# Optimization experiments

Hardware: AMD Instinct MI355X
Metric: run time of the kernel (lower is better)

Reference implementation:

```python
import jax, jax.numpy as jnp
import numpy as np

D_MODEL = 1024
HEADS = 16
D_HEAD = D_MODEL // HEADS
CAUSAL = True


def setup_inputs() -> dict:
    key = jax.random.key(0)
    ks = jax.random.split(key, 11)
    B, L = 4, 2048
    s = 1.0 / np.sqrt(D_MODEL)
    inp = {
        'q': jax.random.normal(ks[0], (B, L, D_MODEL), jnp.float32),
        'k': jax.random.normal(ks[1], (B, L, D_MODEL), jnp.float32),
        'v': jax.random.normal(ks[2], (B, L, D_MODEL), jnp.float32),
        'Wq': jax.random.normal(ks[3], (D_MODEL, D_MODEL), jnp.float32) * s,
        'bq': jnp.zeros((D_MODEL,), jnp.float32),
        'Wk': jax.random.normal(ks[4], (D_MODEL, D_MODEL), jnp.float32) * s,
        'bk': jnp.zeros((D_MODEL,), jnp.float32),
        'Wv': jax.random.normal(ks[5], (D_MODEL, D_MODEL), jnp.float32) * s,
        'bv': jnp.zeros((D_MODEL,), jnp.float32),
        'Wo': jax.random.normal(ks[6], (D_MODEL, D_MODEL), jnp.float32) * s,
        'bo': jnp.zeros((D_MODEL,), jnp.float32),
    }
    return inp


def _split(x):
    B, L, _ = x.shape
    return x.reshape(B, L, HEADS, D_HEAD).transpose(0, 2, 1, 3)  # [B,H,L,Dh]


def reference(q, k, v, Wq, bq, Wk, bk, Wv, bv, Wo, bo):
    qh = _split(q @ Wq + bq)
    kh = _split(k @ Wk + bk)
    vh = _split(v @ Wv + bv)
    scores = jnp.einsum('bhqd,bhkd->bhqk', qh, kh) / jnp.sqrt(jnp.float32(D_HEAD))
    if CAUSAL:
        Lq, Lk = q.shape[1], k.shape[1]
        mask = jnp.triu(jnp.ones((Lq, Lk), bool), k=1)
        scores = jnp.where(mask[None, None], -jnp.inf, scores)
    attn = jax.nn.softmax(scores, axis=-1)
    out = jnp.einsum('bhqk,bhkd->bhqd', attn, vh)
    B, H, L, Dh = out.shape
    out = out.transpose(0, 2, 1, 3).reshape(B, L, H * Dh)
    return out @ Wo + bo
```

## Files before the change

kernel.cpp:

```cpp
#include <hip/hip_runtime.h>

#define DM 1024
#define HEADS 16
#define DH 64
#define BB 4
#define LL 2048
#define MROWS (BB * LL)

typedef __bf16 bf16x8 __attribute__((ext_vector_type(8)));
typedef float f32x4 __attribute__((ext_vector_type(4)));
typedef float f32x16 __attribute__((ext_vector_type(16)));

__device__ __forceinline__ unsigned short f2bf(float f) {
  __bf16 h = (__bf16)f;
  return __builtin_bit_cast(unsigned short, h);
}
__device__ __forceinline__ unsigned int pack2(float a, float b) {
  return (unsigned int)f2bf(a) | ((unsigned int)f2bf(b) << 16);
}

__device__ __forceinline__ void gload16(const unsigned short* g, unsigned short* l) {
  __builtin_amdgcn_global_load_lds(
      (const __attribute__((address_space(1))) unsigned int*)(const void*)g,
      (__attribute__((address_space(3))) unsigned int*)(void*)l, 16, 0, 0);
}

__global__ __launch_bounds__(256) void transpose_w_kernel(
    const float* __restrict__ W0, const float* __restrict__ W1,
    const float* __restrict__ W2, const float* __restrict__ W3,
    unsigned short* __restrict__ T0, unsigned short* __restrict__ T1,
    unsigned short* __restrict__ T2, unsigned short* __restrict__ T3) {
  const float* Wt[4] = {W0, W1, W2, W3};
  unsigned short* Tt[4] = {T0, T1, T2, T3};
  const float* W = Wt[blockIdx.z];
  unsigned short* WT = Tt[blockIdx.z];
  __shared__ float tile[32][33];
  const int tx = threadIdx.x & 31;
  const int ty = threadIdx.x >> 5;
  const int x0 = blockIdx.x * 32;
  const int y0 = blockIdx.y * 32;
#pragma unroll
  for (int i = 0; i < 32; i += 8)
    tile[ty + i][tx] = W[(size_t)(y0 + ty + i) * DM + x0 + tx];
  __syncthreads();
#pragma unroll
  for (int i = 0; i < 32; i += 8)
    WT[(size_t)(x0 + ty + i) * DM + y0 + tx] = f2bf(tile[tx][ty + i]);
}

__global__ __launch_bounds__(256) void cvt_bf16_kernel(
    const float* __restrict__ x, unsigned short* __restrict__ y) {
  const size_t i = ((size_t)blockIdx.x * 256 + threadIdx.x) * 8;
  float4 a = *(const float4*)(x + i);
  float4 b = *(const float4*)(x + i + 4);
  uint4 p = {pack2(a.x, a.y), pack2(a.z, a.w), pack2(b.x, b.y), pack2(b.z, b.w)};
  *(uint4*)(y + i) = p;
}

__global__ __launch_bounds__(256) void cvt3_bf16_kernel(
    const float* __restrict__ q, const float* __restrict__ k,
    const float* __restrict__ v, unsigned short* __restrict__ Xq,
    unsigned short* __restrict__ Xk, unsigned short* __restrict__ Xv) {
  const int z = blockIdx.y;
  const float* x = (z == 0) ? q : (z == 1) ? k : v;
  unsigned short* y = (z == 0) ? Xq : (z == 1) ? Xk : Xv;
  const size_t i = ((size_t)blockIdx.x * 256 + threadIdx.x) * 8;
  float4 a = *(const float4*)(x + i);
  float4 b = *(const float4*)(x + i + 4);
  uint4 p = {pack2(a.x, a.y), pack2(a.z, a.w), pack2(b.x, b.y), pack2(b.z, b.w)};
  *(uint4*)(y + i) = p;
}

template <int OUTMODE>
__device__ __forceinline__ void gemm_body64(
    const unsigned short* __restrict__ A, const unsigned short* __restrict__ BT,
    const float* __restrict__ bias, void* __restrict__ Cptr, float scale) {
  constexpr int K = DM, N = DM;
  __shared__ unsigned short As[128 * 64];
  __shared__ unsigned short Bs[128 * 64];
  const int t = threadIdx.x;
  const int lane = t & 63;
  const int w = t >> 6;
  const int wr = w >> 1, wc = w & 1;
  const int fr = lane & 15, kg = lane >> 4;

  const int flat = blockIdx.y * gridDim.x + blockIdx.x;
  const int cpx = (gridDim.x * gridDim.y) >> 3;
  const int swz = (flat & 7) * cpx + (flat >> 3);
  const int m0 = (swz / gridDim.x) * 128;
  const int n0 = (swz % gridDim.x) * 128;

  const int srow = t >> 3, scol = (t & 7) * 8;

  f32x4 acc[4][4] = {};

  for (int kt = 0; kt < K / 64; ++kt) {
    const int k0 = kt * 64;
#pragma unroll
    for (int i = 0; i < 4; i++) {
      gload16(A + (size_t)(m0 + i * 32 + srow) * K + k0 + scol,
              &As[(i * 256 + t) * 8]);
      gload16(BT + (size_t)(n0 + i * 32 + srow) * K + k0 + scol,
              &Bs[(i * 256 + t) * 8]);
    }
    __syncthreads();

#pragma unroll
    for (int ks = 0; ks < 2; ks++) {
      bf16x8 af[4], bfr[4];
#pragma unroll
      for (int i = 0; i < 4; i++)
        af[i] = *(const bf16x8*)&As[(wr * 64 + i * 16 + fr) * 64 + ks * 32 + kg * 8];
#pragma unroll
      for (int i = 0; i < 4; i++)
        bfr[i] = *(const bf16x8*)&Bs[(wc * 64 + i * 16 + fr) * 64 + ks * 32 + kg * 8];
#pragma unroll
      for (int i = 0; i < 4; i++)
#pragma unroll
        for (int j = 0; j < 4; j++)
          acc[i][j] = __builtin_amdgcn_mfma_f32_16x16x32_bf16(af[i], bfr[j], acc[i][j], 0, 0, 0);
    }
    __syncthreads();
  }

#pragma unroll
  for (int j = 0; j < 4; j++) {
    const int gcol = n0 + wc * 64 + j * 16 + fr;
    const float bv = bias[gcol];
    const int h = gcol >> 6, dh = gcol & 63;
#pragma unroll
    for (int i = 0; i < 4; i++) {
      const int grow0 = m0 + wr * 64 + i * 16 + kg * 4;
      if (OUTMODE == 2) {
        const int b = grow0 >> 11, l = grow0 & 2047;
        uint2 pk;
        pk.x = pack2(acc[i][j][0] + bv, acc[i][j][1] + bv);
        pk.y = pack2(acc[i][j][2] + bv, acc[i][j][3] + bv);
        *(uint2*)((unsigned short*)Cptr +
                  ((size_t)((b * HEADS + h) * DH + dh)) * LL + l) = pk;
      } else {
#pragma unroll
        for (int r = 0; r < 4; r++) {
          const int grow2 = grow0 + r;
          if (OUTMODE == 0) {
            const float val = (acc[i][j][r] + bv) * scale;
            const int b = grow2 >> 11, l = grow2 & 2047;
            ((unsigned short*)Cptr)[(((size_t)(b * HEADS + h) * LL + l) << 6) + dh] = f2bf(val);
          } else {
            ((float*)Cptr)[(size_t)grow2 * N + gcol] = acc[i][j][r] + bv;
          }
        }
      }
    }
  }
}

#define QSCALE 0.18033688011112042f

__global__ __launch_bounds__(256) void qkv_gemm_kernel(
    const unsigned short* __restrict__ A0, size_t strideA,
    const unsigned short* __restrict__ WT0,
    const float* __restrict__ bq, const float* __restrict__ bk,
    const float* __restrict__ bv, unsigned short* __restrict__ O0, int zoff) {
  const int z = (int)blockIdx.z + zoff;
  const unsigned short* A = A0 + (size_t)z * strideA;
  const unsigned short* BT = WT0 + (size_t)z * DM * DM;
  const float* bias = (z == 0) ? bq : (z == 1) ? bk : bv;
  unsigned short* C = O0 + (size_t)z * MROWS * DM;
  if (z == 2)
    gemm_body64<2>(A, BT, bias, C, 1.0f);
  else
    gemm_body64<0>(A, BT, bias, C, (z == 0) ? QSCALE : 1.0f);
}

__global__ __launch_bounds__(256) void oproj_gemm_kernel(
    const unsigned short* __restrict__ Oc, const unsigned short* __restrict__ WoT,
    const float* __restrict__ bo, float* __restrict__ out) {
  gemm_body64<1>(Oc, WoT, bo, out, 1.0f);
}

#define PAD 76
__global__ __launch_bounds__(256, 4) void attn_kernel(
    const unsigned short* __restrict__ Qh, const unsigned short* __restrict__ Kh,
    const unsigned short* __restrict__ VhT, unsigned short* __restrict__ O) {
  __shared__ unsigned short Ks[2][64][PAD];
  __shared__ unsigned short VTs[2][64][PAD];
  const int t = threadIdx.x, lane = t & 63, w = t >> 6;
  const int lo5 = lane & 31, hi = lane >> 5;

  const int f = (int)(blockIdx.y * gridDim.x + blockIdx.x);
  const int l = f >> 8;
  const int c = f & 255;
  const int xcd = c & 7, j = c >> 3;
  const int bh = xcd * 8 + (j & 7);
  const int sub = j >> 3;
  const int qi = (l == 0) ? sub : (l == 1) ? 7 - sub : (l == 2) ? 8 + sub : 15 - sub;

  const size_t base = (size_t)bh * LL * DH;
  const unsigned short* Kb = Kh + base;
  const unsigned short* Vb = VhT + base;

  const int rA = t >> 3, kA = (t & 7) * 8;
  const int rB = rA + 32;

  const int b = bh >> 4, h = bh & 15;

  const int q0 = qi * 128;
  const int qrow = q0 + w * 32 + lo5;

  bf16x8 qf[4];
  {
    const unsigned short* Qb = Qh + base + (size_t)qrow * DH + hi * 8;
#pragma unroll
    for (int kc = 0; kc < 4; kc++) qf[kc] = *(const bf16x8*)(Qb + kc * 16);
  }

  float m_run = -INFINITY, l_run = 0.f;
  f32x16 oacc[2] = {};

  const int ntiles = 2 * (qi + 1);
  const int my_last = (q0 + w * 32 + 31) >> 6;

  uint4 kr0 = *(const uint4*)(Kb + (size_t)rA * DH + kA);
  uint4 kr1 = *(const uint4*)(Kb + (size_t)rB * DH + kA);
  uint4 vr0 = *(const uint4*)(Vb + (size_t)rA * LL + kA);
  uint4 vr1 = *(const uint4*)(Vb + (size_t)rB * LL + kA);
  *(uint4*)&Ks[0][rA][kA] = kr0;
  *(uint4*)&Ks[0][rB][kA] = kr1;
  *(uint4*)&VTs[0][rA][kA] = vr0;
  *(uint4*)&VTs[0][rB][kA] = vr1;

  for (int jt = 0; jt < ntiles; ++jt) {
    const int cur = jt & 1;
    if (jt + 1 < ntiles) {
      const int kv1 = (jt + 1) * 64;
      kr0 = *(const uint4*)(Kb + (size_t)(kv1 + rA) * DH + kA);
      kr1 = *(const uint4*)(Kb + (size_t)(kv1 + rB) * DH + kA);
      vr0 = *(const uint4*)(Vb + (size_t)rA * LL + kv1 + kA);
      vr1 = *(const uint4*)(Vb + (size_t)rB * LL + kv1 + kA);
    }
    __syncthreads();

    if (jt <= my_last) {
      f32x16 s2[2] = {};
      __builtin_amdgcn_s_setprio(1);
#pragma unroll
      for (int tt = 0; tt < 2; tt++)
#pragma unroll
        for (int kc = 0; kc < 4; kc++) {
          bf16x8 kf = *(const bf16x8*)&Ks[cur][tt * 32 + lo5][kc * 16 + hi * 8];
          s2[tt] = __builtin_amdgcn_mfma_f32_32x32x16_bf16(kf, qf[kc], s2[tt], 0, 0, 0);
        }
      __builtin_amdgcn_s_setprio(0);

      const int kv0 = jt * 64;
      if (kv0 + 63 > q0 + w * 32) {
        const int thr = qrow - kv0 - 4 * hi;
#pragma unroll
        for (int tt = 0; tt < 2; tt++)
#pragma unroll
          for (int i = 0; i < 16; i++) {
            const int kvoff = tt * 32 + (i & 3) + 8 * (i >> 2);
            s2[tt][i] = (kvoff > thr) ? -1e30f : s2[tt][i];
          }
      }

      float mx;
      {
        float m8[8];
#pragma unroll
        for (int i = 0; i < 8; i++)
          m8[i] = fmaxf(fmaxf(s2[0][i], s2[0][i + 8]), fmaxf(s2[1][i], s2[1][i + 8]));
        const float a3 = fmaxf(fmaxf(m8[0], m8[1]), m8[2]);
        const float b3 = fmaxf(fmaxf(m8[3], m8[4]), m8[5]);
        const float c3 = fmaxf(m8[6], m8[7]);
        mx = fmaxf(fmaxf(a3, b3), c3);
      }
      mx = fmaxf(mx, __shfl_xor(mx, 32));

      if (__any(mx > m_run + 8.0f)) {
        const float mnew = fmaxf(m_run, mx);
        const float corr = __builtin_amdgcn_exp2f(m_run - mnew);
        m_run = mnew;
        l_run *= corr;
#pragma unroll
        for (int od = 0; od < 2; od++)
#pragma unroll
          for (int i = 0; i < 16; i++) oacc[od][i] *= corr;
      }

#pragma unroll
      for (int tt = 0; tt < 2; tt++)
#pragma unroll
        for (int i = 0; i < 16; i++)
          s2[tt][i] = __builtin_amdgcn_exp2f(s2[tt][i] - m_run);

      float rs;
      {
        float a8[8];
#pragma unroll
        for (int i = 0; i < 8; i++)
          a8[i] = (s2[0][i] + s2[0][i + 8]) + (s2[1][i] + s2[1][i + 8]);
#pragma unroll
        for (int st = 4; st > 0; st >>= 1)
#pragma unroll
          for (int i = 0; i < st; i++) a8[i] += a8[i + st];
        rs = a8[0];
      }
      rs += __shfl_xor(rs, 32);
      l_run += rs;

      union U8 { uint4 u; bf16x8 v; } pa[4];
#pragma unroll
      for (int ks = 0; ks < 4; ks++) {
        const int tt = ks >> 1, b0 = (ks & 1) * 8;
        const unsigned int w0 = pack2(s2[tt][b0 + 0], s2[tt][b0 + 1]);
        const unsigned int w1 = pack2(s2[tt][b0 + 2], s2[tt][b0 + 3]);
        const unsigned int w2 = pack2(s2[tt][b0 + 4], s2[tt][b0 + 5]);
        const unsigned int w3 = pack2(s2[tt][b0 + 6], s2[tt][b0 + 7]);
        const unsigned int p0 = (unsigned int)__shfl_xor((int)w0, 32);
        const unsigned int p1 = (unsigned int)__shfl_xor((int)w1, 32);
        const unsigned int p2 = (unsigned int)__shfl_xor((int)w2, 32);
        const unsigned int p3 = (unsigned int)__shfl_xor((int)w3, 32);
        pa[ks].u = hi ? make_uint4(p2, p3, w2, w3) : make_uint4(w0, w1, p0, p1);
      }

      __builtin_amdgcn_s_setprio(1);
#pragma unroll
      for (int od = 0; od < 2; od++)
#pragma unroll
        for (int ks = 0; ks < 4; ks++) {
          bf16x8 vf = *(const bf16x8*)&VTs[cur][od * 32 + lo5][ks * 16 + hi * 8];
          oacc[od] = __builtin_amdgcn_mfma_f32_32x32x16_bf16(vf, pa[ks].v, oacc[od], 0, 0, 0);
        }
      __builtin_amdgcn_s_setprio(0);
    }

    if (jt + 1 < ntiles) {
      *(uint4*)&Ks[cur ^ 1][rA][kA] = kr0;
      *(uint4*)&Ks[cur ^ 1][rB][kA] = kr1;
      *(uint4*)&VTs[cur ^ 1][rA][kA] = vr0;
      *(uint4*)&VTs[cur ^ 1][rB][kA] = vr1;
    }
  }

  const float linv = 1.f / l_run;
  unsigned short* Ob = O + ((size_t)(b * LL + qrow) * DM) + h * DH;
#pragma unroll
  for (int od = 0; od < 2; od++)
#pragma unroll
    for (int m = 0; m < 8; m++) {
      const int dh0 = od * 32 + ((2 * m) & 3) + 8 * ((2 * m) >> 2) + 4 * hi;
      const unsigned int pk =
          pack2(oacc[od][2 * m] * linv, oacc[od][2 * m + 1] * linv);
      *(unsigned int*)(Ob + dh0) = pk;
    }
}

extern "C" void kernel_launch(void* const* d_in, const int* in_sizes, int n_in,
                              void* d_out, int out_size, void* d_ws, size_t ws_size,
                              hipStream_t stream) {
  (void)in_sizes; (void)n_in; (void)out_size;
  const float* q  = (const float*)d_in[0];
  const float* k  = (const float*)d_in[1];
  const float* v  = (const float*)d_in[2];
  const float* Wq = (const float*)d_in[3];
  const float* bq = (const float*)d_in[4];
  const float* Wk = (const float*)d_in[5];
  const float* bk = (const float*)d_in[6];
  const float* Wv = (const float*)d_in[7];
  const float* bv = (const float*)d_in[8];
  const float* Wo = (const float*)d_in[9];
  const float* bo = (const float*)d_in[10];

  char* ws = (char*)d_ws;
  const size_t WSZ = (size_t)DM * DM * 2;
  const size_t HSZ = (size_t)MROWS * DM * 2;
  unsigned short* WT0 = (unsigned short*)(ws);
  unsigned short* WoT = (unsigned short*)(ws + 3 * WSZ);
  unsigned short* Qh  = (unsigned short*)(ws + 4 * WSZ);
  unsigned short* Kh  = (unsigned short*)(ws + 4 * WSZ + HSZ);
  unsigned short* VhT = (unsigned short*)(ws + 4 * WSZ + 2 * HSZ);
  unsigned short* X   = (unsigned short*)(ws + 4 * WSZ + 3 * HSZ);
  unsigned short* Oc  = X;

  transpose_w_kernel<<<dim3(32, 32, 4), 256, 0, stream>>>(
      Wq, Wk, Wv, Wo,
      WT0, WT0 + DM * DM, WT0 + 2 * (size_t)DM * DM, WoT);

  const dim3 cgrid(MROWS * DM / (256 * 8));
  const dim3 ggrid(DM / 128, MROWS / 128);
  const size_t NEED = 4 * WSZ + 6 * HSZ;

  if (ws_size >= NEED) {
    unsigned short* Xq = X;
    unsigned short* Xk = X + (size_t)MROWS * DM;
    unsigned short* Xv = X + 2 * (size_t)MROWS * DM;
    cvt3_bf16_kernel<<<dim3(MROWS * DM / (256 * 8), 3), 256, 0, stream>>>(
        q, k, v, Xq, Xk, Xv);
    qkv_gemm_kernel<<<dim3(DM / 128, MROWS / 128, 3), 256, 0, stream>>>(
        Xq, (size_t)MROWS * DM, WT0, bq, bk, bv, Qh, 0);
  } else {
    cvt_bf16_kernel<<<cgrid, 256, 0, stream>>>(q, X);
    qkv_gemm_kernel<<<ggrid, 256, 0, stream>>>(X, 0, WT0, bq, bk, bv, Qh, 0);
    cvt_bf16_kernel<<<cgrid, 256, 0, stream>>>(k, X);
    qkv_gemm_kernel<<<ggrid, 256, 0, stream>>>(X, 0, WT0, bq, bk, bv, Qh, 1);
    cvt_bf16_kernel<<<cgrid, 256, 0, stream>>>(v, X);
    qkv_gemm_kernel<<<ggrid, 256, 0, stream>>>(X, 0, WT0, bq, bk, bv, Qh, 2);
  }

  attn_kernel<<<dim3(16, BB * HEADS), 256, 0, stream>>>(Qh, Kh, VhT, Oc);

  oproj_gemm_kernel<<<ggrid, 256, 0, stream>>>(Oc, WoT, bo, (float*)d_out);
}
```

Baseline: 213.9 us.

## Read K/V directly from global in attention and shrink GEMM K-tile to 32

The attention kernel drops its shared-memory double buffer for K and V. Each wave now loads its MFMA operands straight from global memory and loops only up to its own causal limit, so there are no block-wide barriers, and occupancy is raised to 8 blocks per CU. The shared GEMM body is changed from a 64-wide to a 32-wide K tile with a different load mapping. This halves LDS use but doubles the number of barriers per GEMM. The attention change trades LDS traffic and synchronisation for repeated, less coalesced global and L2 reads of K/V by every wave.

```diff
diff --git a/kernel.cpp b/kernel.cpp
--- a/kernel.cpp
+++ b/kernel.cpp
@@ -72,12 +72,12 @@
 }
 
 template <int OUTMODE>
-__device__ __forceinline__ void gemm_body64(
+__device__ __forceinline__ void gemm_body32(
     const unsigned short* __restrict__ A, const unsigned short* __restrict__ BT,
     const float* __restrict__ bias, void* __restrict__ Cptr, float scale) {
   constexpr int K = DM, N = DM;
-  __shared__ unsigned short As[128 * 64];
-  __shared__ unsigned short Bs[128 * 64];
+  __shared__ unsigned short As[128 * 32];
+  __shared__ unsigned short Bs[128 * 32];
   const int t = threadIdx.x;
   const int lane = t & 63;
   const int w = t >> 6;
@@ -90,36 +90,33 @@
   const int m0 = (swz / gridDim.x) * 128;
   const int n0 = (swz % gridDim.x) * 128;
 
-  const int srow = t >> 3, scol = (t & 7) * 8;
+  const int grow = lane >> 2, gcol8 = (lane & 3) * 8;
 
   f32x4 acc[4][4] = {};
 
-  for (int kt = 0; kt < K / 64; ++kt) {
-    const int k0 = kt * 64;
-#pragma unroll
-    for (int i = 0; i < 4; i++) {
-      gload16(A + (size_t)(m0 + i * 32 + srow) * K + k0 + scol,
-              &As[(i * 256 + t) * 8]);
-      gload16(BT + (size_t)(n0 + i * 32 + srow) * K + k0 + scol,
-              &Bs[(i * 256 + t) * 8]);
+  for (int kt = 0; kt < K / 32; ++kt) {
+    const int k0 = kt * 32;
+#pragma unroll
+    for (int i = 0; i < 2; i++) {
+      gload16(A + (size_t)(m0 + i * 64 + w * 16 + grow) * K + k0 + gcol8,
+              &As[(i * 256 + w * 64 + lane) * 8]);
+      gload16(BT + (size_t)(n0 + i * 64 + w * 16 + grow) * K + k0 + gcol8,
+              &Bs[(i * 256 + w * 64 + lane) * 8]);
     }
     __syncthreads();
 
-#pragma unroll
-    for (int ks = 0; ks < 2; ks++) {
-      bf16x8 af[4], bfr[4];
-#pragma unroll
-      for (int i = 0; i < 4; i++)
-        af[i] = *(const bf16x8*)&As[(wr * 64 + i * 16 + fr) * 64 + ks * 32 + kg * 8];
-#pragma unroll
-      for (int i = 0; i < 4; i++)
-        bfr[i] = *(const bf16x8*)&Bs[(wc * 64 + i * 16 + fr) * 64 + ks * 32 + kg * 8];
-#pragma unroll
-      for (int i = 0; i < 4; i++)
-#pragma unroll
-        for (int j = 0; j < 4; j++)
-          acc[i][j] = __builtin_amdgcn_mfma_f32_16x16x32_bf16(af[i], bfr[j], acc[i][j], 0, 0, 0);
-    }
+    bf16x8 af[4], bfr[4];
+#pragma unroll
+    for (int i = 0; i < 4; i++)
+      af[i] = *(const bf16x8*)&As[(wr * 64 + i * 16 + fr) * 32 + kg * 8];
+#pragma unroll
+    for (int i = 0; i < 4; i++)
+      bfr[i] = *(const bf16x8*)&Bs[(wc * 64 + i * 16 + fr) * 32 + kg * 8];
+#pragma unroll
+    for (int i = 0; i < 4; i++)
+#pragma unroll
+      for (int j = 0; j < 4; j++)
+        acc[i][j] = __builtin_amdgcn_mfma_f32_16x16x32_bf16(af[i], bfr[j], acc[i][j], 0, 0, 0);
     __syncthreads();
   }
 
@@ -168,23 +165,20 @@
   const float* bias = (z == 0) ? bq : (z == 1) ? bk : bv;
   unsigned short* C = O0 + (size_t)z * MROWS * DM;
   if (z == 2)
-    gemm_body64<2>(A, BT, bias, C, 1.0f);
+    gemm_body32<2>(A, BT, bias, C, 1.0f);
   else
-    gemm_body64<0>(A, BT, bias, C, (z == 0) ? QSCALE : 1.0f);
+    gemm_body32<0>(A, BT, bias, C, (z == 0) ? QSCALE : 1.0f);
 }
 
 __global__ __launch_bounds__(256) void oproj_gemm_kernel(
     const unsigned short* __restrict__ Oc, const unsigned short* __restrict__ WoT,
     const float* __restrict__ bo, float* __restrict__ out) {
-  gemm_body64<1>(Oc, WoT, bo, out, 1.0f);
-}
-
-#define PAD 76
-__global__ __launch_bounds__(256, 4) void attn_kernel(
+  gemm_body32<1>(Oc, WoT, bo, out, 1.0f);
+}
+
+__global__ __launch_bounds__(256, 8) void attn_kernel(
     const unsigned short* __restrict__ Qh, const unsigned short* __restrict__ Kh,
     const unsigned short* __restrict__ VhT, unsigned short* __restrict__ O) {
-  __shared__ unsigned short Ks[2][64][PAD];
-  __shared__ unsigned short VTs[2][64][PAD];
   const int t = threadIdx.x, lane = t & 63, w = t >> 6;
   const int lo5 = lane & 31, hi = lane >> 5;
 
@@ -200,11 +194,7 @@
   const unsigned short* Kb = Kh + base;
   const unsigned short* Vb = VhT + base;
 
-  const int rA = t >> 3, kA = (t & 7) * 8;
-  const int rB = rA + 32;
-
   const int b = bh >> 4, h = bh & 15;
-
   const int q0 = qi * 128;
   const int qrow = q0 + w * 32 + lo5;
 
@@ -218,130 +208,104 @@
   float m_run = -INFINITY, l_run = 0.f;
   f32x16 oacc[2] = {};
 
-  const int ntiles = 2 * (qi + 1);
   const int my_last = (q0 + w * 32 + 31) >> 6;
 
-  uint4 kr0 = *(const uint4*)(Kb + (size_t)rA * DH + kA);
-  uint4 kr1 = *(const uint4*)(Kb + (size_t)rB * DH + kA);
-  uint4 vr0 = *(const uint4*)(Vb + (size_t)rA * LL + kA);
-  uint4 vr1 = *(const uint4*)(Vb + (size_t)rB * LL + kA);
-  *(uint4*)&Ks[0][rA][kA] = kr0;
-  *(uint4*)&Ks[0][rB][kA] = kr1;
-  *(uint4*)&VTs[0][rA][kA] = vr0;
-  *(uint4*)&VTs[0][rB][kA] = vr1;
-
-  for (int jt = 0; jt < ntiles; ++jt) {
-    const int cur = jt & 1;
-    if (jt + 1 < ntiles) {
-      const int kv1 = (jt + 1) * 64;
-      kr0 = *(const uint4*)(Kb + (size_t)(kv1 + rA) * DH + kA);
-      kr1 = *(const uint4*)(Kb + (size_t)(kv1 + rB) * DH + kA);
-      vr0 = *(const uint4*)(Vb + (size_t)rA * LL + kv1 + kA);
-      vr1 = *(const uint4*)(Vb + (size_t)rB * LL + kv1 + kA);
-    }
-    __syncthreads();
-
-    if (jt <= my_last) {
-      f32x16 s2[2] = {};
-      __builtin_amdgcn_s_setprio(1);
+  for (int jt = 0; jt <= my_last; ++jt) {
+    const int kv0 = jt * 64;
+
+    f32x16 s2[2] = {};
+    __builtin_amdgcn_s_setprio(1);
+#pragma unroll
+    for (int tt = 0; tt < 2; tt++)
+#pragma unroll
+      for (int kc = 0; kc < 4; kc++) {
+        bf16x8 kf = *(const bf16x8*)(Kb + (size_t)(kv0 + tt * 32 + lo5) * DH +
+                                     kc * 16 + hi * 8);
+        s2[tt] = __builtin_amdgcn_mfma_f32_32x32x16_bf16(kf, qf[kc], s2[tt], 0, 0, 0);
+      }
+    __builtin_amdgcn_s_setprio(0);
+
+    if (kv0 + 63 > q0 + w * 32) {
+      const int thr = qrow - kv0 - 4 * hi;
 #pragma unroll
       for (int tt = 0; tt < 2; tt++)
 #pragma unroll
-        for (int kc = 0; kc < 4; kc++) {
-          bf16x8 kf = *(const bf16x8*)&Ks[cur][tt * 32 + lo5][kc * 16 + hi * 8];
-          s2[tt] = __builtin_amdgcn_mfma_f32_32x32x16_bf16(kf, qf[kc], s2[tt], 0, 0, 0);
+        for (int i = 0; i < 16; i++) {
+          const int kvoff = tt * 32 + (i & 3) + 8 * (i >> 2);
+          s2[tt][i] = (kvoff > thr) ? -1e30f : s2[tt][i];
         }
-      __builtin_amdgcn_s_setprio(0);
-
-      const int kv0 = jt * 64;
-      if (kv0 + 63 > q0 + w * 32) {
-        const int thr = qrow - kv0 - 4 * hi;
-#pragma unroll
-        for (int tt = 0; tt < 2; tt++)
-#pragma unroll
-          for (int i = 0; i < 16; i++) {
-            const int kvoff = tt * 32 + (i & 3) + 8 * (i >> 2);
-            s2[tt][i] = (kvoff > thr) ? -1e30f : s2[tt][i];
-          }
+    }
+
+    float mx;
+    {
+      float m8[8];
+#pragma unroll
+      for (int i = 0; i < 8; i++)
+        m8[i] = fmaxf(fmaxf(s2[0][i], s2[0][i + 8]), fmaxf(s2[1][i], s2[1][i + 8]));
+      const float a3 = fmaxf(fmaxf(m8[0], m8[1]), m8[2]);
+      const float b3 = fmaxf(fmaxf(m8[3], m8[4]), m8[5]);
+      const float c3 = fmaxf(m8[6], m8[7]);
+      mx = fmaxf(fmaxf(a3, b3), c3);
+    }
+    mx = fmaxf(mx, __shfl_xor(mx, 32));
+
+    if (__any(mx > m_run + 8.0f)) {
+      const float mnew = fmaxf(m_run, mx);
+      const float corr = __builtin_amdgcn_exp2f(m_run - mnew);
+      m_run = mnew;
+      l_run *= corr;
+#pragma unroll
+      for (int od = 0; od < 2; od++)
+#pragma unroll
+        for (int i = 0; i < 16; i++) oacc[od][i] *= corr;
+    }
+
+#pragma unroll
+    for (int tt = 0; tt < 2; tt++)
+#pragma unroll
+      for (int i = 0; i < 16; i++)
+        s2[tt][i] = __builtin_amdgcn_exp2f(s2[tt][i] - m_run);
+
+    float rs;
+    {
+      float a8[8];
+#pragma unroll
+      for (int i = 0; i < 8; i++)
+        a8[i] = (s2[0][i] + s2[0][i + 8]) + (s2[1][i] + s2[1][i + 8]);
+#pragma unroll
+      for (int st = 4; st > 0; st >>= 1)
+#pragma unroll
+        for (int i = 0; i < st; i++) a8[i] += a8[i + st];
+      rs = a8[0];
+    }
+    rs += __shfl_xor(rs, 32);
+    l_run += rs;
+
+    union U8 { uint4 u; bf16x8 v; } pa[4];
+#pragma unroll
+    for (int ks = 0; ks < 4; ks++) {
+      const int tt = ks >> 1, b0 = (ks & 1) * 8;
+      const unsigned int w0 = pack2(s2[tt][b0 + 0], s2[tt][b0 + 1]);
+      const unsigned int w1 = pack2(s2[tt][b0 + 2], s2[tt][b0 + 3]);
+      const unsigned int w2 = pack2(s2[tt][b0 + 4], s2[tt][b0 + 5]);
+      const unsigned int w3 = pack2(s2[tt][b0 + 6], s2[tt][b0 + 7]);
+      const unsigned int p0 = (unsigned int)__shfl_xor((int)w0, 32);
+      const unsigned int p1 = (unsigned int)__shfl_xor((int)w1, 32);
+      const unsigned int p2 = (unsigned int)__shfl_xor((int)w2, 32);
+      const unsigned int p3 = (unsigned int)__shfl_xor((int)w3, 32);
+      pa[ks].u = hi ? make_uint4(p2, p3, w2, w3) : make_uint4(w0, w1, p0, p1);
+    }
+
+    __builtin_amdgcn_s_setprio(1);
+#pragma unroll
+    for (int od = 0; od < 2; od++)
+#pragma unroll
+      for (int ks = 0; ks < 4; ks++) {
+        bf16x8 vf = *(const bf16x8*)(Vb + (size_t)(od * 32 + lo5) * LL +
+                                     kv0 + ks * 16 + hi * 8);
+        oacc[od] = __builtin_amdgcn_mfma_f32_32x32x16_bf16(vf, pa[ks].v, oacc[od], 0, 0, 0);
       }
-
-      float mx;
-      {
-        float m8[8];
-#pragma unroll
-        for (int i = 0; i < 8; i++)
-          m8[i] = fmaxf(fmaxf(s2[0][i], s2[0][i + 8]), fmaxf(s2[1][i], s2[1][i + 8]));
-        const float a3 = fmaxf(fmaxf(m8[0], m8[1]), m8[2]);
-        const float b3 = fmaxf(fmaxf(m8[3], m8[4]), m8[5]);
-        const float c3 = fmaxf(m8[6], m8[7]);
-        mx = fmaxf(fmaxf(a3, b3), c3);
-      }
-      mx = fmaxf(mx, __shfl_xor(mx, 32));
-
-      if (__any(mx > m_run + 8.0f)) {
-        const float mnew = fmaxf(m_run, mx);
-        const float corr = __builtin_amdgcn_exp2f(m_run - mnew);
-        m_run = mnew;
-        l_run *= corr;
-#pragma unroll
-        for (int od = 0; od < 2; od++)
-#pragma unroll
-          for (int i = 0; i < 16; i++) oacc[od][i] *= corr;
-      }
-
-#pragma unroll
-      for (int tt = 0; tt < 2; tt++)
-#pragma unroll
-        for (int i = 0; i < 16; i++)
-          s2[tt][i] = __builtin_amdgcn_exp2f(s2[tt][i] - m_run);
-
-      float rs;
-      {
-        float a8[8];
-#pragma unroll
-        for (int i = 0; i < 8; i++)
-          a8[i] = (s2[0][i] + s2[0][i + 8]) + (s2[1][i] + s2[1][i + 8]);
-#pragma unroll
-        for (int st = 4; st > 0; st >>= 1)
-#pragma unroll
-          for (int i = 0; i < st; i++) a8[i] += a8[i + st];
-        rs = a8[0];
-      }
-      rs += __shfl_xor(rs, 32);
-      l_run += rs;
-
-      union U8 { uint4 u; bf16x8 v; } pa[4];
-#pragma unroll
-      for (int ks = 0; ks < 4; ks++) {
-        const int tt = ks >> 1, b0 = (ks & 1) * 8;
-        const unsigned int w0 = pack2(s2[tt][b0 + 0], s2[tt][b0 + 1]);
-        const unsigned int w1 = pack2(s2[tt][b0 + 2], s2[tt][b0 + 3]);
-        const unsigned int w2 = pack2(s2[tt][b0 + 4], s2[tt][b0 + 5]);
-        const unsigned int w3 = pack2(s2[tt][b0 + 6], s2[tt][b0 + 7]);
-        const unsigned int p0 = (unsigned int)__shfl_xor((int)w0, 32);
-        const unsigned int p1 = (unsigned int)__shfl_xor((int)w1, 32);
-        const unsigned int p2 = (unsigned int)__shfl_xor((int)w2, 32);
-        const unsigned int p3 = (unsigned int)__shfl_xor((int)w3, 32);
-        pa[ks].u = hi ? make_uint4(p2, p3, w2, w3) : make_uint4(w0, w1, p0, p1);
-      }
-
-      __builtin_amdgcn_s_setprio(1);
-#pragma unroll
-      for (int od = 0; od < 2; od++)
-#pragma unroll
-        for (int ks = 0; ks < 4; ks++) {
-          bf16x8 vf = *(const bf16x8*)&VTs[cur][od * 32 + lo5][ks * 16 + hi * 8];
-          oacc[od] = __builtin_amdgcn_mfma_f32_32x32x16_bf16(vf, pa[ks].v, oacc[od], 0, 0, 0);
-        }
-      __builtin_amdgcn_s_setprio(0);
-    }
-
-    if (jt + 1 < ntiles) {
-      *(uint4*)&Ks[cur ^ 1][rA][kA] = kr0;
-      *(uint4*)&Ks[cur ^ 1][rB][kA] = kr1;
-      *(uint4*)&VTs[cur ^ 1][rA][kA] = vr0;
-      *(uint4*)&VTs[cur ^ 1][rB][kA] = vr1;
-    }
+    __builtin_amdgcn_s_setprio(0);
   }
 
   const float linv = 1.f / l_run;
```

Result: slower. 429.6 us (+100.9%).
